# Kernel optimization log

Hardware: AMD Instinct MI355X
Metric: run time of the kernel (lower is better)

The kernel has to match this reference:

```python
import jax, jax.numpy as jnp
import numpy as np
from jax import lax

H = W = 200          # feature map size
STRIDE = 16
IMG_H = IMG_W = H * STRIDE  # 3200
C = 512
A = 9                # 3 scales x 3 aspect ratios
K_PRE = 1000         # pre-NMS topk (hardcoded in module)
K_POST = 100         # post-NMS keep (hardcoded in module)
IOU_TH = 0.7


def make_anchors():
    scales = jnp.array([128.0, 256.0, 512.0], dtype=jnp.float32)
    ratios = jnp.array([0.5, 1.0, 2.0], dtype=jnp.float32)
    hr = jnp.sqrt(ratios)                      # (3,)
    wr = 1.0 / hr
    ws = (wr[:, None] * scales[None, :]).reshape(-1)   # (9,)
    hs = (hr[:, None] * scales[None, :]).reshape(-1)
    base = jnp.stack([-ws / 2, -hs / 2, ws / 2, hs / 2], axis=1)  # (9,4)
    sx = jnp.arange(W, dtype=jnp.float32) * STRIDE
    sy = jnp.arange(H, dtype=jnp.float32) * STRIDE
    gy, gx = jnp.meshgrid(sy, sx, indexing='ij')
    shifts = jnp.stack([gx, gy, gx, gy], axis=-1).reshape(-1, 4)  # (H*W,4)
    return (shifts[:, None, :] + base[None, :, :]).reshape(-1, 4)  # (H*W*A,4)


def decode(anchors, deltas):
    w = anchors[:, 2] - anchors[:, 0]
    h = anchors[:, 3] - anchors[:, 1]
    cx = anchors[:, 0] + 0.5 * w
    cy = anchors[:, 1] + 0.5 * h
    px = deltas[:, 0] * w + cx
    py = deltas[:, 1] * h + cy
    pw = jnp.exp(deltas[:, 2]) * w
    ph = jnp.exp(deltas[:, 3]) * h
    return jnp.stack([px - 0.5 * pw, py - 0.5 * ph, px + 0.5 * pw, py + 0.5 * ph], axis=1)


def clamp_boxes(b):
    return jnp.stack([
        jnp.clip(b[:, 0], 0.0, IMG_W), jnp.clip(b[:, 1], 0.0, IMG_H),
        jnp.clip(b[:, 2], 0.0, IMG_W), jnp.clip(b[:, 3], 0.0, IMG_H)], axis=1)


def nms_keep(boxes, thr):
    # boxes (K_PRE,4) already sorted by descending score (topk output order)
    x1, y1, x2, y2 = boxes[:, 0], boxes[:, 1], boxes[:, 2], boxes[:, 3]
    areas = (x2 - x1) * (y2 - y1)
    idx = jnp.arange(K_PRE)

    def body(i, keep):
        iw = jnp.clip(jnp.minimum(x2[i], x2) - jnp.maximum(x1[i], x1), 0.0)
        ih = jnp.clip(jnp.minimum(y2[i], y2) - jnp.maximum(y1[i], y1), 0.0)
        inter = iw * ih
        iou = inter / (areas[i] + areas - inter)
        supp = (iou > thr) & (idx > i) & keep[i]
        return keep & jnp.logical_not(supp)

    return lax.fori_loop(0, K_PRE, body, jnp.ones(K_PRE, dtype=bool))


def rpn_forward(feat, conv_w, conv_b, cls_w, cls_b, reg_w, reg_b):
    dn = ('NCHW', 'OIHW', 'NCHW')
    x = lax.conv_general_dilated(feat, conv_w, (1, 1), 'SAME', dimension_numbers=dn)
    x = jax.nn.relu(x + conv_b[None, :, None, None])
    cls = lax.conv_general_dilated(x, cls_w, (1, 1), 'SAME', dimension_numbers=dn) + cls_b[None, :, None, None]
    reg = lax.conv_general_dilated(x, reg_w, (1, 1), 'SAME', dimension_numbers=dn) + reg_b[None, :, None, None]
    # (1,A,H,W) -> (H*W*A,)
    cls_logits = cls.transpose(0, 2, 3, 1).reshape(-1)
    # (1,A*4,H,W) -> (H*W*A,4)
    deltas = reg.reshape(1, A, 4, H, W).transpose(0, 3, 4, 1, 2).reshape(-1, 4)
    anchors = make_anchors()
    proposals = decode(anchors, deltas)
    scores = jax.nn.sigmoid(cls_logits)
    top_sc, top_idx = lax.top_k(scores, K_PRE)           # sorted descending
    props = clamp_boxes(proposals[top_idx])
    keep = lax.stop_gradient(nms_keep(props, IOU_TH))    # NMS decision is non-diff
    # kept indices, in score order (stable sort puts kept first, preserving order)
    order = jnp.argsort(jnp.where(keep, 0, 1), stable=True)[:K_POST]
    valid = jnp.arange(K_POST) < jnp.sum(keep)
    out_boxes = jnp.where(valid[:, None], props[order], 0.0)
    out_scores = jnp.where(valid, top_sc[order], 0.0)
    return out_boxes, out_scores


def setup_inputs() -> dict:
    key = jax.random.key(0)
    ks = jax.random.split(key, 7)
    s = 0.02
    return {
        'feat': jax.random.normal(ks[0], (1, C, H, W), dtype=jnp.float32),
        'conv_w': jax.random.normal(ks[1], (C, C, 3, 3), dtype=jnp.float32) * s,
        'conv_b': jnp.zeros((C,), dtype=jnp.float32),
        'cls_w': jax.random.normal(ks[2], (A, C, 1, 1), dtype=jnp.float32) * s,
        'cls_b': jnp.zeros((A,), dtype=jnp.float32),
        'reg_w': jax.random.normal(ks[3], (A * 4, C, 1, 1), dtype=jnp.float32) * s,
        'reg_b': jnp.zeros((A * 4,), dtype=jnp.float32),
    }


def reference(feat, conv_w, conv_b, cls_w, cls_b, reg_w, reg_b):
    return rpn_forward(feat, conv_w, conv_b, cls_w, cls_b, reg_w, reg_b)
```

## Files before the change

### kernel.cpp

```cpp
#include <hip/hip_runtime.h>
#include <stdint.h>

static constexpr int H_ = 200, W_ = 200, HW_ = 40000;
static constexpr int C_ = 512;
static constexpr int NANCH = 360000;
static constexpr int KPRE = 1000;
static constexpr int KPOST = 100;
static constexpr int KSEL = 1400;
static constexpr int PXCAP = 4096;
static constexpr int KSPLIT = 8;
static constexpr int FT = 212;
static constexpr int FP = 202;

typedef __attribute__((ext_vector_type(8))) short bf16x8;
typedef __attribute__((ext_vector_type(4))) float f32x4;

__device__ inline ushort f2bf(float f) {
    unsigned u = __float_as_uint(f);
    u += 0x7FFFu + ((u >> 16) & 1u);
    return (ushort)(u >> 16);
}
__device__ inline float bf2f(ushort h) { return __uint_as_float(((unsigned)h) << 16); }

typedef const __attribute__((address_space(1))) uint32_t gas_u32;
typedef __attribute__((address_space(3))) uint32_t las_u32;
__device__ __forceinline__ void gload_lds16(const void* g, void* l) {
    __builtin_amdgcn_global_load_lds((gas_u32*)(uintptr_t)g, (las_u32*)(uintptr_t)l, 16, 0, 0);
}

__global__ void k_zero_u32(unsigned* __restrict__ p, int n) {
    int i = blockIdx.x * 256 + threadIdx.x;
    if (i < n) p[i] = 0u;
}

__global__ void k_zero_border_t(ushort* __restrict__ feat_t) {
    int t = blockIdx.x * 256 + threadIdx.x;
    int total = 4944 * 64;
    if (t >= total) return;
    int px = t >> 6, part = t & 63;
    int y, x;
    if (px < 2544) { int ri = px / 212; x = px - ri * 212; y = (ri == 0) ? 0 : 200 + ri; }
    else { int q = px - 2544; int r12 = q / 12; int c = q - r12 * 12; y = 1 + r12; x = (c == 0) ? 0 : 200 + c; }
    uint4 z = {0u, 0u, 0u, 0u};
    *(uint4*)&feat_t[((size_t)y * FT + x) * 512 + part * 8] = z;
}

__global__ void k_zero_border_px(float* __restrict__ feat_px) {
    int t = blockIdx.x * 256 + threadIdx.x;
    int total = 804 * 128;
    if (t >= total) return;
    int px = t >> 7, part = t & 127;
    int y, x;
    if (px < 202)      { y = 0;   x = px; }
    else if (px < 404) { y = 201; x = px - 202; }
    else if (px < 604) { x = 0;   y = 1 + (px - 404); }
    else               { x = 201; y = 1 + (px - 604); }
    float4 z = {0.f, 0.f, 0.f, 0.f};
    *(float4*)&feat_px[((size_t)y * FP + x) * 512 + part * 4] = z;
}

__global__ void k_feat_t(const float* __restrict__ feat, ushort* __restrict__ feat_t) {
    __shared__ ushort lt[32 * 8 * 33];
    int x0 = blockIdx.x * 32, y0 = blockIdx.y * 8, ci0 = blockIdx.z * 32;
    int tid = threadIdx.x;
    for (int u = tid; u < 8192; u += 256) {
        int ciL = u >> 8, rem = u & 255;
        int yy = rem >> 5, xx = rem & 31;
        int x = x0 + xx;
        float v = (x < W_) ? feat[(size_t)(ci0 + ciL) * HW_ + (y0 + yy) * W_ + x] : 0.f;
        lt[(ciL * 8 + yy) * 33 + xx] = f2bf(v);
    }
    __syncthreads();
    for (int u = tid; u < 1024; u += 256) {
        int pxu = u >> 2, part = u & 3;
        int yy = pxu >> 5, xx = pxu & 31;
        if (x0 + xx >= W_) continue;
        ushort tmp[8];
#pragma unroll
        for (int k = 0; k < 8; ++k) tmp[k] = lt[((part * 8 + k) * 8 + yy) * 33 + xx];
        *(uint4*)&feat_t[((size_t)(y0 + yy + 1) * FT + (x0 + xx + 1)) * 512 + ci0 + part * 8] =
            *(const uint4*)&tmp[0];
    }
}

__global__ void k_feat_px(const float* __restrict__ feat, float* __restrict__ feat_px) {
    __shared__ float lt[32 * 8 * 33];
    int x0 = blockIdx.x * 32, y0 = blockIdx.y * 8, ci0 = blockIdx.z * 32;
    int tid = threadIdx.x;
    for (int u = tid; u < 8192; u += 256) {
        int ciL = u >> 8, rem = u & 255;
        int yy = rem >> 5, xx = rem & 31;
        int x = x0 + xx;
        float v = (x < W_) ? feat[(size_t)(ci0 + ciL) * HW_ + (y0 + yy) * W_ + x] : 0.f;
        lt[(ciL * 8 + yy) * 33 + xx] = v;
    }
    __syncthreads();
    for (int u = tid; u < 1024; u += 256) {
        int pxu = u >> 2, part = u & 3;
        int yy = pxu >> 5, xx = pxu & 31;
        if (x0 + xx >= W_) continue;
        float tmp[8];
#pragma unroll
        for (int k = 0; k < 8; ++k) tmp[k] = lt[((part * 8 + k) * 8 + yy) * 33 + xx];
        float* dst = &feat_px[((size_t)(y0 + yy + 1) * FP + (x0 + xx + 1)) * 512 + ci0 + part * 8];
        *(float4*)&dst[0] = *(const float4*)&tmp[0];
        *(float4*)&dst[4] = *(const float4*)&tmp[4];
    }
}

__global__ void k_wt_t(const float* __restrict__ conv_w, ushort* __restrict__ wt_t) {
    int i = blockIdx.x * 256 + threadIdx.x;
    if (i >= 9 * 512 * 512) return;
    int tap = i >> 18;
    int rem = i & 262143;
    int co = rem >> 9, ci = rem & 511;
    wt_t[i] = f2bf(conv_w[((size_t)co * 512 + ci) * 9 + tap]);
}

__global__ void k_wt_ex(const float* __restrict__ conv_w, float* __restrict__ wt_ex) {
    __shared__ float t[32][33];
    int kb = blockIdx.x * 32;
    int cb = blockIdx.y * 32;
    int lx = threadIdx.x, ly = threadIdx.y;
    int tap = kb >> 9, ci0 = kb & 511;
    for (int r = ly; r < 32; r += 8)
        t[r][lx] = conv_w[((size_t)(cb + r) * 512 + ci0 + lx) * 9 + tap];
    __syncthreads();
    for (int r = ly; r < 32; r += 8)
        wt_ex[(size_t)(kb + r) * 512 + cb + lx] = t[lx][r];
}

__global__ __launch_bounds__(256)
__attribute__((amdgpu_waves_per_eu(2, 4)))
void k_conv3_mfma(const ushort* __restrict__ feat_t, const ushort* __restrict__ wt_t,
                  const float* __restrict__ bias, ushort* __restrict__ xab) {
    __shared__ ushort halo[18 * 34 * 32];
    __shared__ ushort wtile[9 * 64 * 32];
    int b = blockIdx.x;
    int cot = b & 7;
    int tile = b >> 3;
    int xt = tile % 7, yt = tile / 7;
    int x0 = xt * 32, y0 = yt * 16;
    int co0 = cot * 64;
    int tid = threadIdx.x;
    int lane = tid & 63, wid = tid >> 6;
    int l15 = lane & 15, l4 = lane >> 4;

    f32x4 acc[4][2][4];
#pragma unroll
    for (int i = 0; i < 4; ++i)
#pragma unroll
        for (int h = 0; h < 2; ++h)
#pragma unroll
            for (int j = 0; j < 4; ++j) acc[i][h][j] = (f32x4){0.f, 0.f, 0.f, 0.f};

    for (int ch = 0; ch < 16; ++ch) {
        int ci0 = ch * 32;
        __syncthreads();
        for (int u = tid; u < 2448; u += 256) {
            int p = u >> 2, q = u & 3;
            int r = p / 34, c = p - r * 34;
            const ushort* src = feat_t + ((size_t)(y0 + r) * FT + (x0 + c)) * 512 + ci0 + q * 8;
            gload_lds16(src, &halo[(u & ~63) * 8]);
        }
        for (int u = tid; u < 2304; u += 256) {
            int row = u >> 2, q = u & 3;
            int tap = row >> 6, co = row & 63;
            const ushort* src = wt_t + ((size_t)(tap * 512 + co0 + co)) * 512 + ci0 + q * 8;
            gload_lds16(src, &wtile[(u & ~63) * 8]);
        }
        __syncthreads();
#pragma unroll
        for (int tap = 0; tap < 9; ++tap) {
            int th = tap / 3, tw = tap - th * 3;
            bf16x8 af[4][2];
#pragma unroll
            for (int pi = 0; pi < 4; ++pi)
#pragma unroll
                for (int xh = 0; xh < 2; ++xh)
                    af[pi][xh] = *(const bf16x8*)&halo[
                        ((wid * 4 + pi + th) * 34 + (xh * 16 + l15 + tw)) * 32 + l4 * 8];
#pragma unroll
            for (int cj = 0; cj < 4; ++cj) {
                bf16x8 bf = *(const bf16x8*)&wtile[(tap * 64 + cj * 16 + l15) * 32 + l4 * 8];
#pragma unroll
                for (int pi = 0; pi < 4; ++pi)
#pragma unroll
                    for (int xh = 0; xh < 2; ++xh)
                        acc[pi][xh][cj] = __builtin_amdgcn_mfma_f32_16x16x32_bf16(
                            af[pi][xh], bf, acc[pi][xh][cj], 0, 0, 0);
            }
        }
    }

    float bv[4];
#pragma unroll
    for (int cj = 0; cj < 4; ++cj) bv[cj] = bias[co0 + cj * 16 + l15];
#pragma unroll
    for (int pi = 0; pi < 4; ++pi) {
        int yy = y0 + wid * 4 + pi;
        if (yy >= H_) continue;
#pragma unroll
        for (int xh = 0; xh < 2; ++xh) {
#pragma unroll
            for (int cj = 0; cj < 4; ++cj) {
                int co = co0 + cj * 16 + l15;
#pragma unroll
                for (int r = 0; r < 4; ++r) {
                    int xx = x0 + xh * 16 + l4 * 4 + r;
                    if (xx < W_) {
                        float v = acc[pi][xh][cj][r] + bv[cj];
                        xab[((size_t)(yy * W_ + xx)) * 512 + co] = f2bf(v > 0.f ? v : 0.f);
                    }
                }
            }
        }
    }
}

__global__ void k_cls(const ushort* __restrict__ xab, const float* __restrict__ cls_w,
                      const float* __restrict__ cls_b, float* __restrict__ scores) {
    __shared__ float wl[9 * 512];
    int tid = threadIdx.x;
    for (int t = tid; t < 4608; t += 256) wl[t] = cls_w[t];
    __syncthreads();
    int l = tid & 63, w = tid >> 6;
    int pbase = blockIdx.x * 64 + w * 16;
    for (int u = 0; u < 16; ++u) {
        int px = pbase + u;
        float xv[8];
#pragma unroll
        for (int k = 0; k < 8; ++k) xv[k] = bf2f(xab[(size_t)px * 512 + k * 64 + l]);
#pragma unroll
        for (int a = 0; a < 9; ++a) {
            float s = 0.f;
#pragma unroll
            for (int k = 0; k < 8; ++k) s = fmaf(xv[k], wl[a * 512 + k * 64 + l], s);
#pragma unroll
            for (int o = 32; o > 0; o >>= 1) s += __shfl_down(s, o);
            if (l == 0) scores[(size_t)px * 9 + a] = 1.f / (1.f + expf(-(s + cls_b[a])));
        }
    }
}

__global__ void k_hist1_lds(const float* __restrict__ scores, unsigned* __restrict__ hist) {
    __shared__ unsigned h[16384];
    int tid = threadIdx.x;
    for (int j = tid; j < 16384; j += 256) h[j] = 0u;
    __syncthreads();
    int stride = gridDim.x * 256;
    for (int i = blockIdx.x * 256 + tid; i < NANCH; i += stride)
        atomicAdd(&h[(__float_as_uint(scores[i]) >> 16) & 16383], 1u);
    __syncthreads();
    for (int j = tid; j < 16384; j += 256) {
        unsigned v = h[j];
        if (v) atomicAdd(&hist[j], v);
    }
}

__global__ void k_find_thr(const unsigned* __restrict__ hist, unsigned* __restrict__ meta,
                           int mode, int Kwant) {
    __shared__ unsigned csum[1024];
    int t = threadIdx.x;
    unsigned base = (mode == 0) ? 0u : meta[1];
    unsigned s = 0;
    for (int b = 0; b < 64; ++b) s += hist[t * 64 + b];
    csum[t] = s;
    __syncthreads();
    for (int off = 1; off < 1024; off <<= 1) {
        unsigned add = (t + off < 1024) ? csum[t + off] : 0u;
        __syncthreads();
        csum[t] += add;
        __syncthreads();
    }
    unsigned run = base + ((t < 1023) ? csum[t + 1] : 0u);
    for (int b = 63; b >= 0; --b) {
        unsigned h = hist[t * 64 + b];
        if (run < (unsigned)Kwant && run + h >= (unsigned)Kwant) {
            if (mode == 0) {
                meta[0] = (unsigned)(t * 64 + b);
                meta[1] = run;
            } else {
                meta[2] = (meta[0] << 16) | (unsigned)(t * 64 + b);
                meta[3] = run;
                meta[4] = (unsigned)Kwant - run;
            }
            break;
        }
        run += h;
    }
}

__global__ void k_collect_cand(const float* __restrict__ scores, const unsigned* __restrict__ meta,
                               unsigned* __restrict__ flags) {
    int i = blockIdx.x * 256 + threadIdx.x;
    if (i >= NANCH) return;
    if ((__float_as_uint(scores[i]) >> 16) >= meta[0]) flags[i / 9] = 1u;
}

__global__ void k_px_compact(unsigned* __restrict__ flags, unsigned* __restrict__ meta,
                             unsigned* __restrict__ px_list) {
    int px = blockIdx.x * 256 + threadIdx.x;
    if (px >= HW_) return;
    if (flags[px]) {
        unsigned s = atomicAdd(&meta[10], 1u);
        if (s < (unsigned)PXCAP) { px_list[s] = (unsigned)px; flags[px] = s + 1u; }
        else flags[px] = 0u;
    }
}

__global__ __attribute__((amdgpu_waves_per_eu(2, 4)))
void k_exact_gemm(const float* __restrict__ feat_px, const float* __restrict__ wt_ex,
                  const unsigned* __restrict__ meta, const unsigned* __restrict__ px_list,
                  float* __restrict__ xpart) {
    int npx = (int)meta[10]; if (npx > PXCAP) npx = PXCAP;
    int pb = blockIdx.x;
    if (pb * 64 >= npx) return;
    int cot = blockIdx.y;
    int kz = blockIdx.z;
    __shared__ float A[32][68];
    __shared__ float B[32][68];
    __shared__ int plist[64];
    int tid = threadIdx.x;
    int co0 = cot * 64;
    if (tid < 64) {
        int slot = pb * 64 + tid;
        plist[tid] = (slot < npx) ? (int)px_list[slot] : (int)px_list[0];
    }
    int tcog = tid >> 4;
    int tpxg = tid & 15;
    float acc[4][4];
#pragma unroll
    for (int i = 0; i < 4; ++i)
#pragma unroll
        for (int j = 0; j < 4; ++j) acc[i][j] = 0.f;
    int kbase = kz * 576;
    for (int kc = 0; kc < 18; ++kc) {
        int k0 = kbase + kc * 32;
        int tap = k0 >> 9, ci0c = k0 & 511;
        int th = tap / 3, tw = tap - th * 3;
        __syncthreads();
        for (int u = tid; u < 512; u += 256) {
            int k = u >> 4, cp = (u & 15) * 4;
            *(float4*)&A[k][cp] = *(const float4*)&wt_ex[(size_t)(k0 + k) * 512 + co0 + cp];
        }
        for (int u = tid; u < 512; u += 256) {
            int s = u >> 3, part = u & 7;
            int px = plist[s];
            int y = px / W_, x = px - y * W_;
            float4 v = *(const float4*)&feat_px[((size_t)(y + th) * FP + (x + tw)) * 512 + ci0c + part * 4];
            B[part * 4 + 0][s] = v.x; B[part * 4 + 1][s] = v.y;
            B[part * 4 + 2][s] = v.z; B[part * 4 + 3][s] = v.w;
        }
        __syncthreads();
#pragma unroll 4
        for (int k = 0; k < 32; ++k) {
            float wv[4], pv[4];
            *(float4*)&wv[0] = *(const float4*)&A[k][tcog * 4];
            *(float4*)&pv[0] = *(const float4*)&B[k][tpxg * 4];
#pragma unroll
            for (int i = 0; i < 4; ++i)
#pragma unroll
                for (int j = 0; j < 4; ++j) acc[i][j] = fmaf(wv[i], pv[j], acc[i][j]);
        }
    }
#pragma unroll
    for (int j = 0; j < 4; ++j) {
        int slot = pb * 64 + tpxg * 4 + j;
        if (slot >= npx) continue;
        f32x4 tmp;
        tmp[0] = acc[0][j]; tmp[1] = acc[1][j]; tmp[2] = acc[2][j]; tmp[3] = acc[3][j];
        __builtin_nontemporal_store(tmp,
            (f32x4*)&xpart[((size_t)kz * PXCAP + slot) * 512 + co0 + tcog * 4]);
    }
}

__global__ void k_exact_reduce(const float* __restrict__ xpart, const float* __restrict__ bias,
                               const unsigned* __restrict__ meta, float* __restrict__ xex) {
    int npx = (int)meta[10]; if (npx > PXCAP) npx = PXCAP;
    int idx = blockIdx.x * 256 + threadIdx.x;
    int slot = idx >> 9, co = idx & 511;
    if (slot >= npx) return;
    float v = 0.f;
#pragma unroll
    for (int kz = 0; kz < KSPLIT; ++kz)
        v += __builtin_nontemporal_load(&xpart[((size_t)kz * PXCAP + slot) * 512 + co]);
    v += bias[co];
    xex[(size_t)slot * 512 + co] = v > 0.f ? v : 0.f;
}

__global__ void k_exact_scores(const float* __restrict__ xex, const float* __restrict__ cls_w,
                               const float* __restrict__ cls_b, const unsigned* __restrict__ meta,
                               float* __restrict__ scores_ex) {
    int slot = blockIdx.x;
    int npx = (int)meta[10]; if (npx > PXCAP) npx = PXCAP;
    if (slot >= npx) return;
    int l = threadIdx.x;
    float xv[8];
#pragma unroll
    for (int k = 0; k < 8; ++k) xv[k] = xex[(size_t)slot * 512 + k * 64 + l];
#pragma unroll
    for (int a = 0; a < 9; ++a) {
        float s = 0.f;
#pragma unroll
        for (int k = 0; k < 8; ++k) s = fmaf(xv[k], cls_w[a * 512 + k * 64 + l], s);
#pragma unroll
        for (int o = 32; o > 0; o >>= 1) s += __shfl_down(s, o);
        if (l == 0) scores_ex[slot * 9 + a] = 1.f / (1.f + expf(-(s + cls_b[a])));
    }
}

__global__ void k_hist1_ex_lds(const float* __restrict__ scores_ex, const unsigned* __restrict__ meta,
                               unsigned* __restrict__ hist) {
    __shared__ unsigned h[16384];
    int npx = (int)meta[10]; if (npx > PXCAP) npx = PXCAP;
    int n = npx * 9;
    int tid = threadIdx.x;
    for (int j = tid; j < 16384; j += 256) h[j] = 0u;
    __syncthreads();
    for (int i = blockIdx.x * 256 + tid; i < n; i += 32 * 256)
        atomicAdd(&h[(__float_as_uint(scores_ex[i]) >> 16) & 16383], 1u);
    __syncthreads();
    for (int j = tid; j < 16384; j += 256) {
        unsigned v = h[j];
        if (v) atomicAdd(&hist[j], v);
    }
}

__global__ void k_hist2_ex(const float* __restrict__ scores_ex, const unsigned* __restrict__ meta,
                           const unsigned* __restrict__ meta_ex, unsigned* __restrict__ hist2) {
    int npx = (int)meta[10]; if (npx > PXCAP) npx = PXCAP;
    int i = blockIdx.x * 256 + threadIdx.x;
    if (i >= npx * 9) return;
    unsigned b = __float_as_uint(scores_ex[i]);
    if ((b >> 16) == meta_ex[0]) atomicAdd(&hist2[b & 0xFFFFu], 1u);
}

__global__ void k_collect_ex(const float* __restrict__ scores_ex, const unsigned* __restrict__ meta,
                             unsigned* __restrict__ meta_ex, const unsigned* __restrict__ px_list,
                             unsigned* __restrict__ sel_bits, unsigned* __restrict__ sel_idx,
                             unsigned* __restrict__ eq_idx) {
    int npx = (int)meta[10]; if (npx > PXCAP) npx = PXCAP;
    int i = blockIdx.x * 256 + threadIdx.x;
    if (i >= npx * 9) return;
    unsigned b = __float_as_uint(scores_ex[i]);
    unsigned T = meta_ex[2];
    unsigned g = px_list[i / 9] * 9u + (unsigned)(i % 9);
    if (b > T) {
        unsigned s = atomicAdd(&meta_ex[8], 1u);
        if (s < 1024u) { sel_bits[s] = b; sel_idx[s] = g; }
    } else if (b == T) {
        unsigned s = atomicAdd(&meta_ex[9], 1u);
        if (s < 65536u) eq_idx[s] = g;
    }
}

__global__ void k_topk_final(const unsigned* __restrict__ sel_bits, const unsigned* __restrict__ sel_idx,
                             const unsigned* __restrict__ eq_idx, const unsigned* __restrict__ meta,
                             unsigned* __restrict__ top_idx, float* __restrict__ top_sc) {
    __shared__ uint64_t keys[1024];
    __shared__ int lcnt;
    __shared__ int lred;
    int t = threadIdx.x;
    unsigned cntGt = meta[3];
    unsigned need = meta[4];
    unsigned cntEq = meta[9];
    unsigned T = meta[2];

    unsigned idx_cut = 0xFFFFFFFFu;
    if (cntEq > need) {
        unsigned lo = 0, hi = NANCH - 1;
        while (lo < hi) {
            unsigned mid = (lo + hi) >> 1;
            int c = 0;
            for (unsigned e = t; e < cntEq; e += 1024)
                if (eq_idx[e] <= mid) c++;
            if (t == 0) lred = 0;
            __syncthreads();
            atomicAdd(&lred, c);
            __syncthreads();
            int tot = lred;
            __syncthreads();
            if ((unsigned)tot >= need) hi = mid; else lo = mid + 1;
        }
        idx_cut = lo;
    }

    keys[t] = 0ull;
    if (t == 0) lcnt = 0;
    __syncthreads();
    for (unsigned s = t; s < cntGt; s += 1024)
        keys[s] = ((uint64_t)sel_bits[s] << 32) | (uint64_t)(0xFFFFFFFFu - sel_idx[s]);
    for (unsigned e = t; e < cntEq; e += 1024) {
        unsigned ix = eq_idx[e];
        if (ix <= idx_cut) {
            int s2 = (int)cntGt + atomicAdd(&lcnt, 1);
            keys[s2] = ((uint64_t)T << 32) | (uint64_t)(0xFFFFFFFFu - ix);
        }
    }
    __syncthreads();
    for (int k = 2; k <= 1024; k <<= 1) {
        for (int j = k >> 1; j > 0; j >>= 1) {
            int ixj = t ^ j;
            if (ixj > t) {
                uint64_t a = keys[t], b = keys[ixj];
                bool desc = (t & k) == 0;
                if (desc ? (a < b) : (a > b)) { keys[t] = b; keys[ixj] = a; }
            }
            __syncthreads();
        }
    }
    if (t < KPRE) {
        top_sc[t] = __uint_as_float((unsigned)(keys[t] >> 32));
        top_idx[t] = 0xFFFFFFFFu - (unsigned)keys[t];
    }
}

__global__ void k_decode(const float* __restrict__ xex, const unsigned* __restrict__ flags,
                         const float* __restrict__ reg_w, const float* __restrict__ reg_b,
                         const unsigned* __restrict__ top_idx,
                         float* __restrict__ props, float* __restrict__ areas) {
    int j = blockIdx.x;
    int lane = threadIdx.x;
    unsigned idx = top_idx[j];
    int pix = (int)(idx / 9u);
    int a = (int)(idx - (unsigned)pix * 9u);
    int slot = (int)flags[pix] - 1;
    if (slot < 0) slot = 0;
    const float* xr = xex + (size_t)slot * 512;
    float s0 = 0, s1 = 0, s2 = 0, s3 = 0;
    for (int c = lane; c < C_; c += 64) {
        float xv = xr[c];
        s0 = fmaf(xv, reg_w[(a * 4 + 0) * C_ + c], s0);
        s1 = fmaf(xv, reg_w[(a * 4 + 1) * C_ + c], s1);
        s2 = fmaf(xv, reg_w[(a * 4 + 2) * C_ + c], s2);
        s3 = fmaf(xv, reg_w[(a * 4 + 3) * C_ + c], s3);
    }
#pragma unroll
    for (int o = 32; o > 0; o >>= 1) {
        s0 += __shfl_down(s0, o);
        s1 += __shfl_down(s1, o);
        s2 += __shfl_down(s2, o);
        s3 += __shfl_down(s3, o);
    }
    if (lane == 0) {
        float d0 = s0 + reg_b[a * 4 + 0];
        float d1 = s1 + reg_b[a * 4 + 1];
        float d2 = s2 + reg_b[a * 4 + 2];
        float d3 = s3 + reg_b[a * 4 + 3];
        int h = pix / W_, w2 = pix - h * W_;
        int rr = a / 3, ss = a - rr * 3;
        float ratio = (rr == 0) ? 0.5f : (rr == 1) ? 1.0f : 2.0f;
        float scale = (ss == 0) ? 128.f : (ss == 1) ? 256.f : 512.f;
        float hr = sqrtf(ratio);
        float wr = 1.0f / hr;
        float wsc = wr * scale, hsc = hr * scale;
        float sx = (float)w2 * 16.f, sy = (float)h * 16.f;
        float a0 = sx - wsc * 0.5f, a1 = sy - hsc * 0.5f;
        float a2 = sx + wsc * 0.5f, a3 = sy + hsc * 0.5f;
        float bw = a2 - a0, bh = a3 - a1;
        float cx = a0 + 0.5f * bw, cy = a1 + 0.5f * bh;
        float px = d0 * bw + cx, py = d1 * bh + cy;
        float pw = expf(d2) * bw, ph = expf(d3) * bh;
        float b0 = px - 0.5f * pw, b1 = py - 0.5f * ph;
        float b2 = px + 0.5f * pw, b3 = py + 0.5f * ph;
        b0 = fminf(fmaxf(b0, 0.f), 3200.f);
        b1 = fminf(fmaxf(b1, 0.f), 3200.f);
        b2 = fminf(fmaxf(b2, 0.f), 3200.f);
        b3 = fminf(fmaxf(b3, 0.f), 3200.f);
        props[j * 4 + 0] = b0;
        props[j * 4 + 1] = b1;
        props[j * 4 + 2] = b2;
        props[j * 4 + 3] = b3;
        areas[j] = (b2 - b0) * (b3 - b1);
    }
}

__global__ void k_nms_mask(const float* __restrict__ props, const float* __restrict__ areas,
                           unsigned long long* __restrict__ mask, float* __restrict__ out) {
    int i = blockIdx.x;
    int tid = threadIdx.x;
    if (i == 0) {
        for (int t = tid; t < KPOST * 5; t += 256) out[t] = 0.f;
    }
    float x1i = props[i * 4 + 0], y1i = props[i * 4 + 1];
    float x2i = props[i * 4 + 2], y2i = props[i * 4 + 3];
    float ai = areas[i];
#pragma unroll
    for (int k = 0; k < 4; ++k) {
        int j = k * 256 + tid;
        bool sup = false;
        if (j < KPRE && j > i) {
            float iw = fminf(x2i, props[j * 4 + 2]) - fmaxf(x1i, props[j * 4 + 0]);
            float ih = fminf(y2i, props[j * 4 + 3]) - fmaxf(y1i, props[j * 4 + 1]);
            iw = fmaxf(iw, 0.f);
            ih = fmaxf(ih, 0.f);
            float inter = iw * ih;
            float iou = inter / (ai + areas[j] - inter);
            sup = iou > 0.7f;
        }
        unsigned long long b = __ballot(sup);
        int word = k * 4 + (tid >> 6);
        if ((tid & 63) == 0) mask[(size_t)i * 16 + word] = b;
    }
}

__global__ void k_nms_scan_out(const unsigned long long* __restrict__ mask,
                               const float* __restrict__ props, const float* __restrict__ top_sc,
                               float* __restrict__ out) {
    __shared__ int kidx[KPOST];
    __shared__ int nk;
    int lane = threadIdx.x;
    if (lane == 0) {
        unsigned long long k0 = ~0ull, k1 = ~0ull, k2 = ~0ull, k3 = ~0ull;
        unsigned long long k4 = ~0ull, k5 = ~0ull, k6 = ~0ull, k7 = ~0ull;
        unsigned long long k8 = ~0ull, k9 = ~0ull, k10 = ~0ull, k11 = ~0ull;
        unsigned long long k12 = ~0ull, k13 = ~0ull, k14 = ~0ull;
        unsigned long long k15 = (1ull << 40) - 1ull;
        int kept = 0;
#define APPLY_ROW(ii) { const unsigned long long* row = &mask[(size_t)(ii) * 16];          \
        k0 &= ~row[0];  k1 &= ~row[1];  k2 &= ~row[2];  k3 &= ~row[3];                     \
        k4 &= ~row[4];  k5 &= ~row[5];  k6 &= ~row[6];  k7 &= ~row[7];                     \
        k8 &= ~row[8];  k9 &= ~row[9];  k10 &= ~row[10]; k11 &= ~row[11];                  \
        k12 &= ~row[12]; k13 &= ~row[13]; k14 &= ~row[14]; k15 &= ~row[15]; }
#define SCAN_WORD(w, kw) { \
        unsigned long long rem = kw; \
        while (rem) { \
            int b = __builtin_ctzll(rem); \
            kidx[kept++] = (w) * 64 + b; \
            if (kept == KPOST) goto done; \
            APPLY_ROW((w) * 64 + b); \
            rem &= kw; \
            rem &= (b >= 63) ? 0ull : ~((2ull << b) - 1ull); \
        } }
        SCAN_WORD(0, k0)  SCAN_WORD(1, k1)  SCAN_WORD(2, k2)  SCAN_WORD(3, k3)
        SCAN_WORD(4, k4)  SCAN_WORD(5, k5)  SCAN_WORD(6, k6)  SCAN_WORD(7, k7)
        SCAN_WORD(8, k8)  SCAN_WORD(9, k9)  SCAN_WORD(10, k10) SCAN_WORD(11, k11)
        SCAN_WORD(12, k12) SCAN_WORD(13, k13) SCAN_WORD(14, k14) SCAN_WORD(15, k15)
done:
        nk = kept;
#undef SCAN_WORD
#undef APPLY_ROW
    }
    __syncthreads();
    int n = nk;
    for (int t = lane; t < KPOST; t += 64) {
        if (t < n) {
            int i = kidx[t];
            out[t * 4 + 0] = props[i * 4 + 0];
            out[t * 4 + 1] = props[i * 4 + 1];
            out[t * 4 + 2] = props[i * 4 + 2];
            out[t * 4 + 3] = props[i * 4 + 3];
            out[KPOST * 4 + t] = top_sc[i];
        }
    }
}

extern "C" void kernel_launch(void* const* d_in, const int* in_sizes, int n_in,
                              void* d_out, int out_size, void* d_ws, size_t ws_size,
                              hipStream_t stream) {
    const float* feat   = (const float*)d_in[0];
    const float* conv_w = (const float*)d_in[1];
    const float* conv_b = (const float*)d_in[2];
    const float* cls_w  = (const float*)d_in[3];
    const float* cls_b  = (const float*)d_in[4];
    const float* reg_w  = (const float*)d_in[5];
    const float* reg_b  = (const float*)d_in[6];
    float* out = (float*)d_out;

    size_t off = 0;
    auto alloc = [&](size_t bytes) -> void* {
        off = (off + 255) & ~(size_t)255;
        void* p = (char*)d_ws + off;
        off += bytes;
        return p;
    };
    ushort* feat_t  = (ushort*)alloc((size_t)FT * FT * 512 * 2);
    float*  feat_px = (float*)alloc((size_t)FP * FP * 512 * 4);
    ushort* wt_t    = (ushort*)alloc((size_t)9 * 512 * 512 * 2);
    float*  wt_ex   = (float*)alloc((size_t)9 * 512 * 512 * 4);
    ushort* xab     = (ushort*)alloc((size_t)HW_ * 512 * 2);
    float*  xpart   = (float*)alloc((size_t)KSPLIT * PXCAP * 512 * 4);
    float*  xex     = (float*)alloc((size_t)PXCAP * 512 * 4);
    float*  scores  = (float*)alloc((size_t)NANCH * 4);
    float*  scores_ex = (float*)alloc((size_t)PXCAP * 9 * 4);
    unsigned* hist1   = (unsigned*)alloc(65536 * 4);
    unsigned* hist2   = (unsigned*)alloc(65536 * 4);
    unsigned* meta    = (unsigned*)alloc(64 * 4);
    unsigned* meta_ex = (unsigned*)alloc(64 * 4);
    unsigned* flags   = (unsigned*)alloc((size_t)HW_ * 4);
    unsigned* px_list = (unsigned*)alloc(PXCAP * 4);
    unsigned* sel_bits = (unsigned*)alloc(1024 * 4);
    unsigned* sel_idx  = (unsigned*)alloc(1024 * 4);
    unsigned* eq_idx   = (unsigned*)alloc(65536 * 4);
    unsigned* top_idx  = (unsigned*)alloc(KPRE * 4);
    float* top_sc      = (float*)alloc(KPRE * 4);
    float* props       = (float*)alloc(KPRE * 4 * 4);
    float* areas       = (float*)alloc(KPRE * 4);
    unsigned long long* mask = (unsigned long long*)alloc((size_t)KPRE * 16 * 8);
    (void)ws_size; (void)in_sizes; (void)n_in; (void)out_size;

    k_zero_border_t<<<(4944 * 64 + 255) / 256, 256, 0, stream>>>(feat_t);
    int zrDw = 65536 * 2 + 64 + 64 + HW_;
    k_zero_u32<<<(zrDw + 255) / 256, 256, 0, stream>>>(hist1, zrDw);
    k_feat_t<<<dim3(7, 25, 16), 256, 0, stream>>>(feat, feat_t);
    k_wt_t<<<(9 * 512 * 512 + 255) / 256, 256, 0, stream>>>(conv_w, wt_t);
    k_conv3_mfma<<<8 * 91, 256, 0, stream>>>(feat_t, wt_t, conv_b, xab);
    k_cls<<<HW_ / 64, 256, 0, stream>>>(xab, cls_w, cls_b, scores);
    k_hist1_lds<<<64, 256, 0, stream>>>(scores, hist1);
    k_find_thr<<<1, 1024, 0, stream>>>(hist1, meta, 0, KSEL);
    k_collect_cand<<<(NANCH + 255) / 256, 256, 0, stream>>>(scores, meta, flags);
    k_px_compact<<<(HW_ + 255) / 256, 256, 0, stream>>>(flags, meta, px_list);
    k_zero_border_px<<<(804 * 128 + 255) / 256, 256, 0, stream>>>(feat_px);
    k_feat_px<<<dim3(7, 25, 16), 256, 0, stream>>>(feat, feat_px);
    k_wt_ex<<<dim3(144, 16), dim3(32, 8), 0, stream>>>(conv_w, wt_ex);
    k_zero_u32<<<(65536 * 2 + 255) / 256, 256, 0, stream>>>(hist1, 65536 * 2);
    k_exact_gemm<<<dim3(PXCAP / 64, 8, KSPLIT), 256, 0, stream>>>(feat_px, wt_ex, meta, px_list, xpart);
    k_exact_reduce<<<PXCAP * 512 / 256, 256, 0, stream>>>(xpart, conv_b, meta, xex);
    k_exact_scores<<<PXCAP, 64, 0, stream>>>(xex, cls_w, cls_b, meta, scores_ex);
    k_hist1_ex_lds<<<32, 256, 0, stream>>>(scores_ex, meta, hist1);
    k_find_thr<<<1, 1024, 0, stream>>>(hist1, meta_ex, 0, KPRE);
    k_hist2_ex<<<(PXCAP * 9 + 255) / 256, 256, 0, stream>>>(scores_ex, meta, meta_ex, hist2);
    k_find_thr<<<1, 1024, 0, stream>>>(hist2, meta_ex, 1, KPRE);
    k_collect_ex<<<(PXCAP * 9 + 255) / 256, 256, 0, stream>>>(scores_ex, meta, meta_ex, px_list,
                                                              sel_bits, sel_idx, eq_idx);
    k_topk_final<<<1, 1024, 0, stream>>>(sel_bits, sel_idx, eq_idx, meta_ex, top_idx, top_sc);
    k_decode<<<KPRE, 64, 0, stream>>>(xex, flags, reg_w, reg_b, top_idx, props, areas);
    k_nms_mask<<<KPRE, 256, 0, stream>>>(props, areas, mask, out);
    k_nms_scan_out<<<1, 64, 0, stream>>>(mask, props, top_sc, out);
}
```

Baseline: 697.1 us.

## Fuse 1x1 cls projection into conv epilogue, drop bf16 activation tensor

```diff
diff --git a/kernel.cpp b/kernel.cpp
--- a/kernel.cpp
+++ b/kernel.cpp
@@ -133,7 +133,8 @@
 __global__ __launch_bounds__(256)
 __attribute__((amdgpu_waves_per_eu(2, 4)))
 void k_conv3_mfma(const ushort* __restrict__ feat_t, const ushort* __restrict__ wt_t,
-                  const float* __restrict__ bias, ushort* __restrict__ xab) {
+                  const float* __restrict__ bias, const float* __restrict__ cls_w,
+                  float* __restrict__ cls_part) {
     __shared__ ushort halo[18 * 34 * 32];
     __shared__ ushort wtile[9 * 64 * 32];
     int b = blockIdx.x;
@@ -193,54 +194,59 @@
         }
     }
 
+    float clw[9][4];
+#pragma unroll
+    for (int a = 0; a < 9; ++a)
+#pragma unroll
+        for (int cj = 0; cj < 4; ++cj)
+            clw[a][cj] = cls_w[a * 512 + co0 + cj * 16 + l15];
     float bv[4];
 #pragma unroll
     for (int cj = 0; cj < 4; ++cj) bv[cj] = bias[co0 + cj * 16 + l15];
 #pragma unroll
     for (int pi = 0; pi < 4; ++pi) {
         int yy = y0 + wid * 4 + pi;
-        if (yy >= H_) continue;
 #pragma unroll
         for (int xh = 0; xh < 2; ++xh) {
-#pragma unroll
-            for (int cj = 0; cj < 4; ++cj) {
-                int co = co0 + cj * 16 + l15;
+            float xv[4][4];
+#pragma unroll
+            for (int cj = 0; cj < 4; ++cj)
 #pragma unroll
                 for (int r = 0; r < 4; ++r) {
-                    int xx = x0 + xh * 16 + l4 * 4 + r;
-                    if (xx < W_) {
-                        float v = acc[pi][xh][cj][r] + bv[cj];
-                        xab[((size_t)(yy * W_ + xx)) * 512 + co] = f2bf(v > 0.f ? v : 0.f);
-                    }
+                    float v = acc[pi][xh][cj][r] + bv[cj];
+                    xv[cj][r] = v > 0.f ? v : 0.f;
+                }
+#pragma unroll
+            for (int r = 0; r < 4; ++r) {
+                int xx = x0 + xh * 16 + l4 * 4 + r;
+                bool valid = (yy < H_) && (xx < W_);
+#pragma unroll
+                for (int a = 0; a < 9; ++a) {
+                    float s = xv[0][r] * clw[a][0];
+                    s = fmaf(xv[1][r], clw[a][1], s);
+                    s = fmaf(xv[2][r], clw[a][2], s);
+                    s = fmaf(xv[3][r], clw[a][3], s);
+                    s += __shfl_xor(s, 1);
+                    s += __shfl_xor(s, 2);
+                    s += __shfl_xor(s, 4);
+                    s += __shfl_xor(s, 8);
+                    if (valid && l15 == a)
+                        cls_part[(size_t)cot * NANCH + ((size_t)yy * W_ + xx) * 9 + a] = s;
                 }
             }
         }
     }
 }
 
-__global__ void k_cls(const ushort* __restrict__ xab, const float* __restrict__ cls_w,
-                      const float* __restrict__ cls_b, float* __restrict__ scores) {
-    __shared__ float wl[9 * 512];
-    int tid = threadIdx.x;
-    for (int t = tid; t < 4608; t += 256) wl[t] = cls_w[t];
-    __syncthreads();
-    int l = tid & 63, w = tid >> 6;
-    int pbase = blockIdx.x * 64 + w * 16;
-    for (int u = 0; u < 16; ++u) {
-        int px = pbase + u;
-        float xv[8];
-#pragma unroll
-        for (int k = 0; k < 8; ++k) xv[k] = bf2f(xab[(size_t)px * 512 + k * 64 + l]);
-#pragma unroll
-        for (int a = 0; a < 9; ++a) {
-            float s = 0.f;
-#pragma unroll
-            for (int k = 0; k < 8; ++k) s = fmaf(xv[k], wl[a * 512 + k * 64 + l], s);
-#pragma unroll
-            for (int o = 32; o > 0; o >>= 1) s += __shfl_down(s, o);
-            if (l == 0) scores[(size_t)px * 9 + a] = 1.f / (1.f + expf(-(s + cls_b[a])));
-        }
-    }
+__global__ void k_cls_fin(const float* __restrict__ cls_part, const float* __restrict__ cls_b,
+                          float* __restrict__ scores) {
+    int i = blockIdx.x * 256 + threadIdx.x;
+    if (i >= NANCH) return;
+    float s = 0.f;
+#pragma unroll
+    for (int c = 0; c < 8; ++c) s += cls_part[(size_t)c * NANCH + i];
+    int a = i % 9;
+    scores[i] = 1.f / (1.f + expf(-(s + cls_b[a])));
 }
 
 __global__ void k_hist1_lds(const float* __restrict__ scores, unsigned* __restrict__ hist) {
@@ -679,7 +685,7 @@
     float*  feat_px = (float*)alloc((size_t)FP * FP * 512 * 4);
     ushort* wt_t    = (ushort*)alloc((size_t)9 * 512 * 512 * 2);
     float*  wt_ex   = (float*)alloc((size_t)9 * 512 * 512 * 4);
-    ushort* xab     = (ushort*)alloc((size_t)HW_ * 512 * 2);
+    float*  cls_part = (float*)alloc((size_t)8 * NANCH * 4);
     float*  xpart   = (float*)alloc((size_t)KSPLIT * PXCAP * 512 * 4);
     float*  xex     = (float*)alloc((size_t)PXCAP * 512 * 4);
     float*  scores  = (float*)alloc((size_t)NANCH * 4);
@@ -705,8 +711,8 @@
     k_zero_u32<<<(zrDw + 255) / 256, 256, 0, stream>>>(hist1, zrDw);
     k_feat_t<<<dim3(7, 25, 16), 256, 0, stream>>>(feat, feat_t);
     k_wt_t<<<(9 * 512 * 512 + 255) / 256, 256, 0, stream>>>(conv_w, wt_t);
-    k_conv3_mfma<<<8 * 91, 256, 0, stream>>>(feat_t, wt_t, conv_b, xab);
-    k_cls<<<HW_ / 64, 256, 0, stream>>>(xab, cls_w, cls_b, scores);
+    k_conv3_mfma<<<8 * 91, 256, 0, stream>>>(feat_t, wt_t, conv_b, cls_w, cls_part);
+    k_cls_fin<<<(NANCH + 255) / 256, 256, 0, stream>>>(cls_part, cls_b, scores);
     k_hist1_lds<<<64, 256, 0, stream>>>(scores, hist1);
     k_find_thr<<<1, 1024, 0, stream>>>(hist1, meta, 0, KSEL);
     k_collect_cand<<<(NANCH + 255) / 256, 256, 0, stream>>>(scores, meta, flags);
```

Result: no change. 697.5 us (+0.1%).

## Restructure cls head as thread-per-pixel with LDS-staged activations

Applied to the files above, without the earlier changes.

```diff
diff --git a/kernel.cpp b/kernel.cpp
--- a/kernel.cpp
+++ b/kernel.cpp
@@ -220,27 +220,32 @@
 
 __global__ void k_cls(const ushort* __restrict__ xab, const float* __restrict__ cls_w,
                       const float* __restrict__ cls_b, float* __restrict__ scores) {
-    __shared__ float wl[9 * 512];
-    int tid = threadIdx.x;
-    for (int t = tid; t < 4608; t += 256) wl[t] = cls_w[t];
-    __syncthreads();
-    int l = tid & 63, w = tid >> 6;
-    int pbase = blockIdx.x * 64 + w * 16;
-    for (int u = 0; u < 16; ++u) {
-        int px = pbase + u;
+    __shared__ ushort xt[64 * 520];
+    int t = threadIdx.x;
+    int pxb = blockIdx.x * 64;
+    for (int i = 0; i < 64; ++i)
+        *(uint4*)&xt[i * 520 + t * 8] =
+            *(const uint4*)&xab[((size_t)(pxb + i)) * 512 + t * 8];
+    __syncthreads();
+    float acc[9];
+#pragma unroll
+    for (int a = 0; a < 9; ++a) acc[a] = 0.f;
+    const ushort* row = &xt[t * 520];
+    for (int k = 0; k < 64; ++k) {
+        bf16x8 v = *(const bf16x8*)&row[k * 8];
         float xv[8];
 #pragma unroll
-        for (int k = 0; k < 8; ++k) xv[k] = bf2f(xab[(size_t)px * 512 + k * 64 + l]);
-#pragma unroll
-        for (int a = 0; a < 9; ++a) {
-            float s = 0.f;
-#pragma unroll
-            for (int k = 0; k < 8; ++k) s = fmaf(xv[k], wl[a * 512 + k * 64 + l], s);
-#pragma unroll
-            for (int o = 32; o > 0; o >>= 1) s += __shfl_down(s, o);
-            if (l == 0) scores[(size_t)px * 9 + a] = 1.f / (1.f + expf(-(s + cls_b[a])));
-        }
-    }
+        for (int j = 0; j < 8; ++j) xv[j] = bf2f((ushort)v[j]);
+#pragma unroll
+        for (int a = 0; a < 9; ++a)
+#pragma unroll
+            for (int j = 0; j < 8; ++j)
+                acc[a] = fmaf(xv[j], cls_w[a * 512 + k * 8 + j], acc[a]);
+    }
+    int px = pxb + t;
+#pragma unroll
+    for (int a = 0; a < 9; ++a)
+        scores[(size_t)px * 9 + a] = 1.f / (1.f + expf(-(acc[a] + cls_b[a])));
 }
 
 __global__ void k_hist1_lds(const float* __restrict__ scores, unsigned* __restrict__ hist) {
@@ -706,7 +711,7 @@
     k_feat_t<<<dim3(7, 25, 16), 256, 0, stream>>>(feat, feat_t);
     k_wt_t<<<(9 * 512 * 512 + 255) / 256, 256, 0, stream>>>(conv_w, wt_t);
     k_conv3_mfma<<<8 * 91, 256, 0, stream>>>(feat_t, wt_t, conv_b, xab);
-    k_cls<<<HW_ / 64, 256, 0, stream>>>(xab, cls_w, cls_b, scores);
+    k_cls<<<HW_ / 64, 64, 0, stream>>>(xab, cls_w, cls_b, scores);
     k_hist1_lds<<<64, 256, 0, stream>>>(scores, hist1);
     k_find_thr<<<1, 1024, 0, stream>>>(hist1, meta, 0, KSEL);
     k_collect_cand<<<(NANCH + 255) / 256, 256, 0, stream>>>(scores, meta, flags);
```

New measurement: 705.8 us. No clear change (+1.3%).
